# Optimization experiments

Measured on AMD Instinct MI355X. Metric: run time of the kernel, lower is better.

## Reference

```python
import jax, jax.numpy as jnp
import numpy as np

B, ND, NPR, D, H = 8, 512, 1024, 256, 8
DH = D // H
K_T, G_MIN, RHO, B_LAM, TOPK_RATIO, EDL_LAM = 4.0, 1e-4, 0.3, 0.01, 0.5, 1e-3
NEG = -1e30  # stands in for -inf in masked_fill (softmax weight is exactly 0 either way)


def setup_inputs():
    key = jax.random.key(0)
    ks = jax.random.split(key, 20)
    H_D = jax.random.normal(ks[0], (B, ND, D), jnp.float32)
    H_P = jax.random.normal(ks[1], (B, NPR, D), jnp.float32)
    mask_D = (jax.random.uniform(ks[2], (B, ND)) > 0.2).at[:, :2].set(True)
    mask_P = (jax.random.uniform(ks[3], (B, NPR)) > 0.2).at[:, :2].set(True)
    s = 0.02
    p = {
        'nig_w': s * jax.random.normal(ks[4], (D, 4), jnp.float32),
        'nig_b': jnp.zeros((4,), jnp.float32),
        'Wq': s * jax.random.normal(ks[5], (D, D), jnp.float32), 'bq': jnp.zeros((D,), jnp.float32),
        'Wk': s * jax.random.normal(ks[6], (D, D), jnp.float32), 'bk': jnp.zeros((D,), jnp.float32),
        'Wv': s * jax.random.normal(ks[7], (D, D), jnp.float32), 'bv': jnp.zeros((D,), jnp.float32),
        'Wo': s * jax.random.normal(ks[8], (D, D), jnp.float32), 'bo': jnp.zeros((D,), jnp.float32),
        'ln_g': jnp.ones((D,), jnp.float32), 'ln_b': jnp.zeros((D,), jnp.float32),
    }
    return dict(H_D=H_D, mask_D=mask_D, H_P=H_P, mask_P=mask_P, **p)


def _layernorm(x, g, b):
    m = jnp.mean(x, -1, keepdims=True)
    v = jnp.mean((x - m) ** 2, -1, keepdims=True)
    return (x - m) * jax.lax.rsqrt(v + 1e-5) * g + b


def _nig(h, w, b):
    # NIGHead: linear d->4 evidential params; s2 = predictive variance beta/(nu*(alpha-1))
    raw = h @ w + b                               # [B,N,4]
    nu = jax.nn.softplus(raw[..., 1])
    alpha = 1.0 + jax.nn.softplus(raw[..., 2])
    beta = jax.nn.softplus(raw[..., 3])
    s2 = beta / (nu * (alpha - 1.0) + 1e-6)
    return raw[..., 0], nu, alpha, beta, s2


def _apply_topk(g, mask):
    # per-row variable k = floor(clamp(sum(mask)*ratio, min=1)); keep top-k of g, zero rest
    k = jnp.maximum(jnp.sum(mask, axis=1).astype(jnp.float32) * TOPK_RATIO, 1.0).astype(jnp.int32)
    ranks = jnp.argsort(jnp.argsort(-g, axis=1), axis=1)  # rank 0 = largest
    keep = ranks < k[:, None]
    return jnp.where(keep, g, 0.0) * mask.astype(g.dtype)


def _mhca(qx, kx, mask_k, log_g, Wq, bq, Wk, bk, Wv, bv, Wo, bo, ln_g, ln_b):
    Bq, Nq, Dd = qx.shape
    Nk = kx.shape[1]
    q = (qx @ Wq + bq).reshape(Bq, Nq, H, DH).transpose(0, 2, 1, 3)
    k = (kx @ Wk + bk).reshape(Bq, Nk, H, DH).transpose(0, 2, 1, 3)
    v = (kx @ Wv + bv).reshape(Bq, Nk, H, DH).transpose(0, 2, 1, 3)
    attn = jnp.einsum('bhqd,bhkd->bhqk', q, k) / jnp.sqrt(jnp.float32(DH))
    attn = jnp.where(mask_k[:, None, None, :], attn, NEG)
    if log_g is not None:
        attn = attn + log_g[:, None, None, :]
    w = jax.nn.softmax(attn, axis=-1)
    ctx = jnp.einsum('bhqk,bhkd->bhqd', w, v).transpose(0, 2, 1, 3).reshape(Bq, Nq, Dd)
    return _layernorm(ctx @ Wo + bo + qx, ln_g, ln_b)


def reference(H_D, mask_D, H_P, mask_P, nig_w, nig_b, Wq, bq, Wk, bk, Wv, bv, Wo, bo, ln_g, ln_b):
    # stage='B', k_now=None path
    _, _, aD, bD, s2_D = _nig(H_D, nig_w, nig_b)
    _, _, aP, bP, s2_P = _nig(H_P, nig_w, nig_b)
    mDf, mPf = mask_D.astype(jnp.float32), mask_P.astype(jnp.float32)
    # GateFromUncertainty: g = clamp(exp(-k*s2), g_min, 1) * mask
    g_D = _apply_topk(jnp.clip(jnp.exp(-K_T * s2_D), G_MIN, 1.0) * mDf, mask_D)
    g_P = _apply_topk(jnp.clip(jnp.exp(-K_T * s2_P), G_MIN, 1.0) * mPf, mask_P)
    log_g_D, log_g_P = jnp.log(g_D + 1e-8), jnp.log(g_P + 1e-8)
    # BudgetRegularizer: lam*(masked mean gate - rho)^2 ; EDLRegularizer: lam*mean(alpha+beta)
    budget = lambda g, mf: B_LAM * (jnp.sum(g) / (jnp.sum(mf) + 1e-8) - RHO) ** 2
    edl = lambda a, b: EDL_LAM * jnp.mean(a + b)
    loss_reg = budget(g_D, mDf) + budget(g_P, mPf) + edl(aD, bD) + edl(aP, bP)
    mha = (Wq, bq, Wk, bk, Wv, bv, Wo, bo, ln_g, ln_b)
    Xd, Xp = H_D, H_P
    Xd = _mhca(Xd, Xp, mask_P, log_g_P, *mha)
    Xp = _mhca(Xp, Xd, mask_D, log_g_D, *mha)
    return Xd, Xp, g_D, g_P, loss_reg
```

## Files before the change

### kernel.cpp

```cpp
#include <hip/hip_runtime.h>
#include <hip/hip_bf16.h>
#include <math.h>

typedef __attribute__((ext_vector_type(8))) short s8;
typedef __attribute__((ext_vector_type(8))) unsigned short us8;
typedef __attribute__((ext_vector_type(4))) unsigned short us4;
typedef __attribute__((ext_vector_type(4))) float f4;

__device__ __forceinline__ unsigned short f2bf(float f) {
    unsigned int u = __float_as_uint(f);
    unsigned int r = u + 0x7FFFu + ((u >> 16) & 1u);
    return (unsigned short)(r >> 16);
}

__device__ __forceinline__ float softplus_f(float x) {
    return (x > 0.f) ? x + log1pf(expf(-x)) : log1pf(expf(x));
}

__global__ __launch_bounds__(256) void prep_nig_kernel(
        const float* __restrict__ W0, const float* __restrict__ W1,
        const float* __restrict__ W2, const float* __restrict__ W3,
        unsigned short* __restrict__ Wt,
        const float* __restrict__ H_D, const int* __restrict__ maskD,
        const float* __restrict__ H_P, const int* __restrict__ maskP,
        const float* __restrict__ nw, const float* __restrict__ nb,
        float* __restrict__ gpreD, float* __restrict__ gpreP,
        float* __restrict__ abD, float* __restrict__ abP,
        unsigned short* __restrict__ hdb, unsigned short* __restrict__ hpb) {
    int bx = blockIdx.x;
    if (bx < 256) {
        __shared__ float t[32][33];
        int wsel = bx >> 6, tile = bx & 63;
        const float* W = wsel == 0 ? W0 : wsel == 1 ? W1 : wsel == 2 ? W2 : W3;
        unsigned short* O = Wt + wsel * 65536;
        int k0 = (tile >> 3) * 32, n0 = (tile & 7) * 32;
        int r = threadIdx.x >> 5, c = threadIdx.x & 31;
#pragma unroll
        for (int i = 0; i < 4; ++i) t[r + i * 8][c] = W[(k0 + r + i * 8) * 256 + n0 + c];
        __syncthreads();
#pragma unroll
        for (int i = 0; i < 4; ++i) O[(n0 + r + i * 8) * 256 + k0 + c] = f2bf(t[c][r + i * 8]);
        return;
    }
    int row = (bx - 256) * 4 + (threadIdx.x >> 6);
    int lane = threadIdx.x & 63;
    const float* H; const int* mask; float* gpre; float* ab; unsigned short* hb; int lr;
    if (row < 4096) { H = H_D; mask = maskD; gpre = gpreD; ab = abD; hb = hdb; lr = row; }
    else            { H = H_P; mask = maskP; gpre = gpreP; ab = abP; hb = hpb; lr = row - 4096; }
    float4 hv = *(const float4*)(H + (size_t)lr * 256 + lane * 4);
    us4 h4 = { f2bf(hv.x), f2bf(hv.y), f2bf(hv.z), f2bf(hv.w) };
    *(us4*)&hb[(size_t)lr * 256 + lane * 4] = h4;
    float4 n0v = *(const float4*)&nw[(lane * 4 + 0) * 4];
    float4 n1v = *(const float4*)&nw[(lane * 4 + 1) * 4];
    float4 n2v = *(const float4*)&nw[(lane * 4 + 2) * 4];
    float4 n3v = *(const float4*)&nw[(lane * 4 + 3) * 4];
    float a1 = hv.x * n0v.y + hv.y * n1v.y + hv.z * n2v.y + hv.w * n3v.y;
    float a2 = hv.x * n0v.z + hv.y * n1v.z + hv.z * n2v.z + hv.w * n3v.z;
    float a3 = hv.x * n0v.w + hv.y * n1v.w + hv.z * n2v.w + hv.w * n3v.w;
#pragma unroll
    for (int o = 32; o; o >>= 1) {
        a1 += __shfl_xor(a1, o);
        a2 += __shfl_xor(a2, o);
        a3 += __shfl_xor(a3, o);
    }
    if (lane == 0) {
        float nu = softplus_f(a1 + nb[1]);
        float sa = softplus_f(a2 + nb[2]);
        float beta = softplus_f(a3 + nb[3]);
        float s2 = beta / (nu * sa + 1e-6f);
        float g = expf(-4.f * s2);
        g = fminf(fmaxf(g, 1e-4f), 1.f);
        gpre[lr] = (mask[lr] != 0) ? g : 0.f;
        ab[lr] = (1.f + sa) + beta;
    }
}

__device__ __forceinline__ void gemm64x128_lds(
        const unsigned short* __restrict__ Ab, const unsigned short* __restrict__ Wp,
        const float* __restrict__ bias, unsigned short* __restrict__ Cb,
        int idx, unsigned short (*bpan)[5120]) {
    const int tid = threadIdx.x, wid = tid >> 6, lane = tid & 63;
    const int g = lane >> 4, lo = lane & 15;
    const size_t row0 = (size_t)(idx >> 1) * 64 + wid * 16;
    const int n0 = (idx & 1) * 128;
    const int c0 = tid >> 2, q0 = tid & 3;
    const unsigned short* gp0 = Wp + (size_t)(n0 + c0) * 256 + q0 * 8;
    const unsigned short* gp1 = Wp + (size_t)(n0 + c0 + 64) * 256 + q0 * 8;
    const int l0 = c0 * 40 + q0 * 8;
    const int l1 = (c0 + 64) * 40 + q0 * 8;
    const unsigned short* ap = Ab + (row0 + lo) * 256 + g * 8;

    f4 acc[8];
#pragma unroll
    for (int f = 0; f < 8; ++f) acc[f] = (f4){0.f, 0.f, 0.f, 0.f};

    *(us8*)&bpan[0][l0] = *(const us8*)gp0;
    *(us8*)&bpan[0][l1] = *(const us8*)gp1;
    s8 av = *(const s8*)ap;

    for (int t = 0; t < 8; ++t) {
        const int buf = t & 1;
        us8 pn0, pn1; s8 avn;
        if (t < 7) {
            pn0 = *(const us8*)(gp0 + (t + 1) * 32);
            pn1 = *(const us8*)(gp1 + (t + 1) * 32);
            avn = *(const s8*)(ap + (t + 1) * 32);
        }
        __syncthreads();
#pragma unroll
        for (int f = 0; f < 8; ++f) {
            s8 bfr = *(const s8*)&bpan[buf][(f * 16 + lo) * 40 + g * 8];
            acc[f] = __builtin_amdgcn_mfma_f32_16x16x32_bf16(av, bfr, acc[f], 0, 0, 0);
        }
        if (t < 7) {
            *(us8*)&bpan[buf ^ 1][l0] = pn0;
            *(us8*)&bpan[buf ^ 1][l1] = pn1;
            av = avn;
        }
    }
#pragma unroll
    for (int f = 0; f < 8; ++f) {
        int col = n0 + f * 16 + lo;
        float bv2 = bias[col];
#pragma unroll
        for (int r = 0; r < 4; ++r)
            Cb[(row0 + g * 4 + r) * 256 + col] = f2bf(acc[f][r] + bv2);
    }
}

__device__ __forceinline__ void topk_body(
        const float* __restrict__ gpre, const int* __restrict__ mask,
        float* __restrict__ gout, float* __restrict__ logg,
        float* __restrict__ sgArr, float* __restrict__ smArr,
        int N, int b, int by, int bslot, float* grow, float* red) {
    int tid = threadIdx.x;
    int j = by * 256 + tid;
    for (int i = tid; i < N; i += 256) grow[i] = gpre[b * N + i];
    float cpart = 0.f;
    for (int i = tid; i < N; i += 256) cpart += (mask[b * N + i] != 0) ? 1.f : 0.f;
    red[tid] = cpart;
    __syncthreads();
    for (int s = 128; s; s >>= 1) { if (tid < s) red[tid] += red[tid + s]; __syncthreads(); }
    float count = red[0];
    __syncthreads();
    int k = (int)fmaxf(count * 0.5f, 1.0f);
    float gj = grow[j];
    int rank = 0;
    for (int i = 0; i < N; ++i) {
        float gi = grow[i];
        rank += (gi > gj || (gi == gj && i < j)) ? 1 : 0;
    }
    float gf = (rank < k) ? gj : 0.f;
    gout[b * N + j] = gf;
    logg[b * N + j] = logf(gf + 1e-8f);
    red[tid] = gf;
    __syncthreads();
    for (int s = 128; s; s >>= 1) { if (tid < s) red[tid] += red[tid + s]; __syncthreads(); }
    if (tid == 0) sgArr[bslot] = red[0];
    __syncthreads();
    red[tid] = (mask[b * N + j] != 0) ? 1.f : 0.f;
    __syncthreads();
    for (int s = 128; s; s >>= 1) { if (tid < s) red[tid] += red[tid + s]; __syncthreads(); }
    if (tid == 0) smArr[bslot] = red[0];
}

__global__ __launch_bounds__(256) void qkv_topk_kernel(
        const unsigned short* __restrict__ hdb, const unsigned short* __restrict__ hpb,
        const unsigned short* __restrict__ Wt,
        const float* __restrict__ bq, const float* __restrict__ bk, const float* __restrict__ bv,
        unsigned short* __restrict__ q1b, unsigned short* __restrict__ k1b,
        unsigned short* __restrict__ v1b, unsigned short* __restrict__ q2b,
        const float* __restrict__ gpreD, const int* __restrict__ maskD,
        float* __restrict__ goutD, float* __restrict__ loggD,
        const float* __restrict__ gpreP, const int* __restrict__ maskP,
        float* __restrict__ goutP, float* __restrict__ loggP,
        float* __restrict__ sgD, float* __restrict__ smD,
        float* __restrict__ sgP, float* __restrict__ smP,
        const float* __restrict__ abD, const float* __restrict__ abP,
        float* __restrict__ edl2) {
    __shared__ unsigned short bpan[2][5120];
    int bx = blockIdx.x;
    int tid = threadIdx.x;
    if (bx == 944) {
        float* red = (float*)&bpan[0][0];
        float s1 = 0.f, s2 = 0.f;
        for (int i = tid; i < 4096; i += 256) s1 += abD[i];
        for (int i = tid; i < 8192; i += 256) s2 += abP[i];
        red[tid] = s1;
        __syncthreads();
        for (int s = 128; s; s >>= 1) { if (tid < s) red[tid] += red[tid + s]; __syncthreads(); }
        if (tid == 0) edl2[0] = red[0];
        __syncthreads();
        red[tid] = s2;
        __syncthreads();
        for (int s = 128; s; s >>= 1) { if (tid < s) red[tid] += red[tid + s]; __syncthreads(); }
        if (tid == 0) edl2[1] = red[0];
        return;
    }
    if (bx >= 896) {
        float* grow = (float*)&bpan[0][0];
        float* red = grow + 1024;
        int tb = bx - 896;
        int b = tb & 7, by = tb >> 3;
        if (by < 2) topk_body(gpreD, maskD, goutD, loggD, sgD, smD, 512, b, by, b * 2 + by, grow, red);
        else        topk_body(gpreP, maskP, goutP, loggP, sgP, smP, 1024, b, by - 2, b * 4 + (by - 2), grow, red);
        return;
    }
    const unsigned short* Ab; const unsigned short* Wp; const float* bias;
    unsigned short* Cb; int idx;
    if (bx < 128)      { Ab = hdb; Wp = Wt;          bias = bq; Cb = q1b; idx = bx; }
    else if (bx < 384) { Ab = hpb; Wp = Wt + 65536;  bias = bk; Cb = k1b; idx = bx - 128; }
    else if (bx < 640) { Ab = hpb; Wp = Wt + 131072; bias = bv; Cb = v1b; idx = bx - 384; }
    else               { Ab = hpb; Wp = Wt;          bias = bq; Cb = q2b; idx = bx - 640; }
    gemm64x128_lds(Ab, Wp, bias, Cb, idx, bpan);
}

__global__ __launch_bounds__(256) void kv2_mega_kernel(
        const unsigned short* __restrict__ xdb, const unsigned short* __restrict__ Wt,
        const float* __restrict__ bk, const float* __restrict__ bv,
        unsigned short* __restrict__ k2b, unsigned short* __restrict__ v2b) {
    __shared__ unsigned short bpan[2][5120];
    int bx = blockIdx.x;
    const unsigned short* Wp; const float* bias; unsigned short* Cb; int idx;
    if (bx < 128) { Wp = Wt + 65536;  bias = bk; Cb = k2b; idx = bx; }
    else          { Wp = Wt + 131072; bias = bv; Cb = v2b; idx = bx - 128; }
    gemm64x128_lds(xdb, Wp, bias, Cb, idx, bpan);
}

__global__ __launch_bounds__(256) void gemm_o_ln_kernel(
        const unsigned short* __restrict__ A, const unsigned short* __restrict__ Wt,
        const float* __restrict__ bias, const float* __restrict__ resid,
        const float* __restrict__ gam, const float* __restrict__ bet,
        float* __restrict__ Out, unsigned short* __restrict__ OutB,
        const float* __restrict__ sgD, const float* __restrict__ smD,
        const float* __restrict__ sgP, const float* __restrict__ smP,
        const float* __restrict__ edl2, float* __restrict__ lossOut) {
    __shared__ float sums[4][16], sqs[4][16];
    const int tid = threadIdx.x, wid = tid >> 6, lane = tid & 63;
    const int g = lane >> 4, lo = lane & 15;
    const size_t row0 = (size_t)blockIdx.x * 16;
    const int c0 = wid * 64;
    f4 acc[4];
#pragma unroll
    for (int f = 0; f < 4; ++f) acc[f] = (f4){0.f, 0.f, 0.f, 0.f};
    for (int k0 = 0; k0 < 256; k0 += 32) {
        s8 af = *(const s8*)&A[(row0 + lo) * 256 + k0 + g * 8];
#pragma unroll
        for (int f = 0; f < 4; ++f) {
            s8 bfr = *(const s8*)&Wt[(size_t)(c0 + f * 16 + lo) * 256 + k0 + g * 8];
            acc[f] = __builtin_amdgcn_mfma_f32_16x16x32_bf16(af, bfr, acc[f], 0, 0, 0);
        }
    }
#pragma unroll
    for (int r = 0; r < 4; ++r) {
        size_t row = row0 + g * 4 + r;
        float sv = 0.f, qv = 0.f;
#pragma unroll
        for (int f = 0; f < 4; ++f) {
            int col = c0 + f * 16 + lo;
            float v = acc[f][r] + bias[col] + resid[row * 256 + col];
            acc[f][r] = v;
            sv += v;
            qv += v * v;
        }
#pragma unroll
        for (int o = 1; o < 16; o <<= 1) { sv += __shfl_xor(sv, o); qv += __shfl_xor(qv, o); }
        if (lo == 0) { sums[wid][g * 4 + r] = sv; sqs[wid][g * 4 + r] = qv; }
    }
    __syncthreads();
#pragma unroll
    for (int r = 0; r < 4; ++r) {
        int rl = g * 4 + r;
        size_t row = row0 + rl;
        float st = sums[0][rl] + sums[1][rl] + sums[2][rl] + sums[3][rl];
        float qt = sqs[0][rl] + sqs[1][rl] + sqs[2][rl] + sqs[3][rl];
        float mean = st * (1.f / 256.f);
        float var = qt * (1.f / 256.f) - mean * mean;
        float inv = rsqrtf(var + 1e-5f);
#pragma unroll
        for (int f = 0; f < 4; ++f) {
            int col = c0 + f * 16 + lo;
            float y = (acc[f][r] - mean) * inv * gam[col] + bet[col];
            Out[row * 256 + col] = y;
            if (OutB) OutB[row * 256 + col] = f2bf(y);
        }
    }
    if (lossOut && blockIdx.x == 0 && tid < 64) {
        float sgd = 0.f, smd = 0.f, sgp = 0.f, smp = 0.f;
        if (lane < 16) { sgd = sgD[lane]; smd = smD[lane]; }
        if (lane < 32) { sgp = sgP[lane]; smp = smP[lane]; }
#pragma unroll
        for (int o = 16; o; o >>= 1) { sgp += __shfl_xor(sgp, o); smp += __shfl_xor(smp, o); }
#pragma unroll
        for (int o = 8; o; o >>= 1) { sgd += __shfl_xor(sgd, o); smd += __shfl_xor(smd, o); }
        if (lane == 0) {
            float t1 = sgd / (smd + 1e-8f) - 0.3f;
            float t2 = sgp / (smp + 1e-8f) - 0.3f;
            lossOut[0] = 0.01f * (t1 * t1) + 0.01f * (t2 * t2)
                       + 1e-3f * (edl2[0] / 4096.f) + 1e-3f * (edl2[1] / 8192.f);
        }
    }
}

template <int NK>
__global__ __launch_bounds__(256) void attn_mfma_kernel(
        const unsigned short* __restrict__ qb, const unsigned short* __restrict__ kb,
        const unsigned short* __restrict__ vb, const float* __restrict__ logg,
        unsigned short* __restrict__ ctxb, int Nq) {
    __shared__ unsigned short Kf[2][2048];
    __shared__ unsigned short Vf[2][2048];
    __shared__ unsigned short Pf[4][1152];
    __shared__ float lg[2][64];
    constexpr int NT = NK / 64;

    const int tid = threadIdx.x;
    const int wid = tid >> 6, lane = tid & 63;
    const int g = lane >> 4, lo = lane & 15;
    const int b = blockIdx.y >> 3, h = blockIdx.y & 7;
    const int q0 = blockIdx.x * 64 + wid * 16;
    const size_t bq = (size_t)b * Nq, bk = (size_t)b * NK;
    const float scale = 0.17677669529663687f;

    const int kloc = tid >> 2, quad = tid & 3;
    const size_t gbase = (bk + kloc) * 256 + h * 32 + quad * 8;
    const int kfa = ((kloc >> 4) << 9) + (quad * 16 + (kloc & 15)) * 8;
    const int vkh = kloc >> 5, vgg = (kloc >> 3) & 3, vj = kloc & 7;
    const int vdh = quad >> 1, vl0 = (quad & 1) * 8;
    const int vb0 = ((vkh * 2 + vdh) << 9) + vgg * 128 + vj;

    s8 qf = *(const s8*)&qb[(bq + q0 + lo) * 256 + h * 32 + g * 8];

    f4 o0 = {0.f, 0.f, 0.f, 0.f}, o1 = {0.f, 0.f, 0.f, 0.f};
    float mrow[4] = {-3e38f, -3e38f, -3e38f, -3e38f};
    float lsum[4] = {0.f, 0.f, 0.f, 0.f};

    us8 kreg = *(const us8*)&kb[gbase];
    us8 vreg = *(const us8*)&vb[gbase];
    float lgreg = (tid < 64) ? logg[bk + tid] : 0.f;
    *(us8*)&Kf[0][kfa] = kreg;
#pragma unroll
    for (int jj = 0; jj < 8; ++jj) Vf[0][vb0 + (vl0 + jj) * 8] = vreg[jj];
    if (tid < 64) lg[0][tid] = lgreg;

    for (int t = 0; t < NT; ++t) {
        const int cur = t & 1;
        if (t + 1 < NT) {
            size_t ga = gbase + (size_t)(t + 1) * 64 * 256;
            kreg = *(const us8*)&kb[ga];
            vreg = *(const us8*)&vb[ga];
            if (tid < 64) lgreg = logg[bk + (t + 1) * 64 + tid];
        }
        __syncthreads();

        f4 sc[4];
#pragma unroll
        for (int ks = 0; ks < 4; ++ks) {
            s8 kfr = *(const s8*)&Kf[cur][(ks << 9) + lane * 8];
            f4 z = {0.f, 0.f, 0.f, 0.f};
            f4 s4 = __builtin_amdgcn_mfma_f32_16x16x32_bf16(qf, kfr, z, 0, 0, 0);
            float lga = lg[cur][ks * 16 + lo];
#pragma unroll
            for (int r = 0; r < 4; ++r) sc[ks][r] = s4[r] * scale + lga;
        }
        float vm[4];
#pragma unroll
        for (int r = 0; r < 4; ++r)
            vm[r] = fmaxf(fmaxf(sc[0][r], sc[1][r]), fmaxf(sc[2][r], sc[3][r]));
#pragma unroll
        for (int off = 1; off < 16; off <<= 1)
#pragma unroll
            for (int r = 0; r < 4; ++r) vm[r] = fmaxf(vm[r], __shfl_xor(vm[r], off));
        float al[4], ps[4];
#pragma unroll
        for (int r = 0; r < 4; ++r) {
            float mn = fmaxf(mrow[r], vm[r]);
            al[r] = __expf(mrow[r] - mn);
            mrow[r] = mn;
            ps[r] = 0.f;
        }
#pragma unroll
        for (int ks = 0; ks < 4; ++ks)
#pragma unroll
            for (int r = 0; r < 4; ++r) {
                float p = __expf(sc[ks][r] - mrow[r]);
                ps[r] += p;
                Pf[wid][(g * 4 + r) * 72 + ks * 16 + lo] = f2bf(p);
            }
#pragma unroll
        for (int off = 1; off < 16; off <<= 1)
#pragma unroll
            for (int r = 0; r < 4; ++r) ps[r] += __shfl_xor(ps[r], off);
#pragma unroll
        for (int r = 0; r < 4; ++r) {
            lsum[r] = lsum[r] * al[r] + ps[r];
            o0[r] *= al[r];
            o1[r] *= al[r];
        }
#pragma unroll
        for (int kh = 0; kh < 2; ++kh) {
            s8 pfr = *(const s8*)&Pf[wid][lo * 72 + kh * 32 + g * 8];
            s8 vf0 = *(const s8*)&Vf[cur][((kh * 2 + 0) << 9) + lane * 8];
            o0 = __builtin_amdgcn_mfma_f32_16x16x32_bf16(pfr, vf0, o0, 0, 0, 0);
            s8 vf1 = *(const s8*)&Vf[cur][((kh * 2 + 1) << 9) + lane * 8];
            o1 = __builtin_amdgcn_mfma_f32_16x16x32_bf16(pfr, vf1, o1, 0, 0, 0);
        }
        if (t + 1 < NT) {
            const int nxt = cur ^ 1;
            *(us8*)&Kf[nxt][kfa] = kreg;
#pragma unroll
            for (int jj = 0; jj < 8; ++jj) Vf[nxt][vb0 + (vl0 + jj) * 8] = vreg[jj];
            if (tid < 64) lg[nxt][tid] = lgreg;
        }
    }
#pragma unroll
    for (int r = 0; r < 4; ++r) {
        float inv = 1.f / lsum[r];
        unsigned short* cp = ctxb + (bq + q0 + g * 4 + r) * 256 + h * 32;
        cp[lo] = f2bf(o0[r] * inv);
        cp[16 + lo] = f2bf(o1[r] * inv);
    }
}

extern "C" void kernel_launch(void* const* d_in, const int* in_sizes, int n_in,
                              void* d_out, int out_size, void* d_ws, size_t ws_size,
                              hipStream_t stream) {
    (void)in_sizes; (void)n_in; (void)out_size; (void)ws_size;
    const float* H_D   = (const float*)d_in[0];
    const int*   maskD = (const int*)d_in[1];
    const float* H_P   = (const float*)d_in[2];
    const int*   maskP = (const int*)d_in[3];
    const float* nig_w = (const float*)d_in[4];
    const float* nig_b = (const float*)d_in[5];
    const float* Wq = (const float*)d_in[6];
    const float* bq = (const float*)d_in[7];
    const float* Wk = (const float*)d_in[8];
    const float* bk = (const float*)d_in[9];
    const float* Wv = (const float*)d_in[10];
    const float* bv = (const float*)d_in[11];
    const float* Wo = (const float*)d_in[12];
    const float* bo = (const float*)d_in[13];
    const float* ln_g = (const float*)d_in[14];
    const float* ln_b = (const float*)d_in[15];
    float* out = (float*)d_out;
    float* ws = (float*)d_ws;

    float* outXd = out + 0;
    float* outXp = out + 1048576;
    float* outGD = out + 3145728;
    float* outGP = out + 3149824;
    float* outLo = out + 3158016;

    float* abD   = ws;
    float* abP   = ws + 4096;
    float* sgD   = ws + 12288;
    float* smD   = ws + 12304;
    float* sgP   = ws + 12320;
    float* smP   = ws + 12352;
    float* edl2  = ws + 12384;
    float* gpreD = ws + 12416;
    float* gpreP = ws + 16512;
    float* logD  = ws + 24704;
    float* logP  = ws + 28800;
    unsigned short* ub  = (unsigned short*)(ws + 36992);
    unsigned short* Wt  = ub;
    unsigned short* q1b = ub + 262144;
    unsigned short* k1b = ub + 1310720;
    unsigned short* v1b = ub + 3407872;
    unsigned short* q2b = ub + 5505024;
    unsigned short* c1b = ub + 7602176;
    unsigned short* xdb = ub + 8650752;
    unsigned short* k2b = ub + 9699328;
    unsigned short* v2b = ub + 10747904;
    unsigned short* c2b = ub + 11796480;
    unsigned short* hdb = c1b;
    unsigned short* hpb = xdb;

    prep_nig_kernel<<<3328, 256, 0, stream>>>(Wq, Wk, Wv, Wo, Wt,
                                              H_D, maskD, H_P, maskP,
                                              nig_w, nig_b, gpreD, gpreP, abD, abP,
                                              hdb, hpb);
    qkv_topk_kernel<<<945, 256, 0, stream>>>(hdb, hpb, Wt, bq, bk, bv,
                                             q1b, k1b, v1b, q2b,
                                             gpreD, maskD, outGD, logD,
                                             gpreP, maskP, outGP, logP,
                                             sgD, smD, sgP, smP, abD, abP, edl2);
    attn_mfma_kernel<1024><<<dim3(8, 64), 256, 0, stream>>>(q1b, k1b, v1b, logP, c1b, 512);
    gemm_o_ln_kernel<<<256, 256, 0, stream>>>(c1b, Wt + 3 * 65536, bo, H_D, ln_g, ln_b,
                                              outXd, xdb, nullptr, nullptr, nullptr, nullptr,
                                              nullptr, nullptr);
    kv2_mega_kernel<<<256, 256, 0, stream>>>(xdb, Wt, bk, bv, k2b, v2b);
    attn_mfma_kernel<512><<<dim3(16, 64), 256, 0, stream>>>(q2b, k2b, v2b, logD, c2b, 1024);
    gemm_o_ln_kernel<<<512, 256, 0, stream>>>(c2b, Wt + 3 * 65536, bo, H_P, ln_g, ln_b,
                                              outXp, nullptr, sgD, smD, sgP, smP, edl2, outLo);
}
```

Baseline: 140.2 us.

## Fuse Xd output projection+LayerNorm with the K/V projection for the second attention

The first output-projection+LayerNorm kernel now stages its bf16 normalized rows in LDS and immediately computes the K and V projections for the second attention pass from them. This removes one kernel launch and the global write and re-read of the intermediate bf16 Xd buffer. The fused kernel uses only 256 blocks of 16 rows each and reads the Wk/Wv weights directly from global memory per block instead of through the LDS-panelled 64x128 GEMM, so it has less parallelism and more weight traffic.

```diff
diff --git a/kernel.cpp b/kernel.cpp
--- a/kernel.cpp
+++ b/kernel.cpp
@@ -215,23 +215,98 @@
     gemm64x128_lds(Ab, Wp, bias, Cb, idx, bpan);
 }
 
-__global__ __launch_bounds__(256) void kv2_mega_kernel(
-        const unsigned short* __restrict__ xdb, const unsigned short* __restrict__ Wt,
+__global__ __launch_bounds__(256) void gemm_o_ln_kv2_kernel(
+        const unsigned short* __restrict__ A, const unsigned short* __restrict__ Wt,
+        const float* __restrict__ bo, const float* __restrict__ resid,
+        const float* __restrict__ gam, const float* __restrict__ bet,
+        float* __restrict__ Out,
         const float* __restrict__ bk, const float* __restrict__ bv,
         unsigned short* __restrict__ k2b, unsigned short* __restrict__ v2b) {
-    __shared__ unsigned short bpan[2][5120];
-    int bx = blockIdx.x;
-    const unsigned short* Wp; const float* bias; unsigned short* Cb; int idx;
-    if (bx < 128) { Wp = Wt + 65536;  bias = bk; Cb = k2b; idx = bx; }
-    else          { Wp = Wt + 131072; bias = bv; Cb = v2b; idx = bx - 128; }
-    gemm64x128_lds(xdb, Wp, bias, Cb, idx, bpan);
+    __shared__ float sums[4][16], sqs[4][16];
+    __shared__ unsigned short xs[16][264];
+    const int tid = threadIdx.x, wid = tid >> 6, lane = tid & 63;
+    const int g = lane >> 4, lo = lane & 15;
+    const size_t row0 = (size_t)blockIdx.x * 16;
+    const int c0 = wid * 64;
+    const unsigned short* Wo = Wt + 3 * 65536;
+    f4 acc[4];
+#pragma unroll
+    for (int f = 0; f < 4; ++f) acc[f] = (f4){0.f, 0.f, 0.f, 0.f};
+    for (int k0 = 0; k0 < 256; k0 += 32) {
+        s8 af = *(const s8*)&A[(row0 + lo) * 256 + k0 + g * 8];
+#pragma unroll
+        for (int f = 0; f < 4; ++f) {
+            s8 bfr = *(const s8*)&Wo[(size_t)(c0 + f * 16 + lo) * 256 + k0 + g * 8];
+            acc[f] = __builtin_amdgcn_mfma_f32_16x16x32_bf16(af, bfr, acc[f], 0, 0, 0);
+        }
+    }
+#pragma unroll
+    for (int r = 0; r < 4; ++r) {
+        size_t row = row0 + g * 4 + r;
+        float sv = 0.f, qv = 0.f;
+#pragma unroll
+        for (int f = 0; f < 4; ++f) {
+            int col = c0 + f * 16 + lo;
+            float v = acc[f][r] + bo[col] + resid[row * 256 + col];
+            acc[f][r] = v;
+            sv += v;
+            qv += v * v;
+        }
+#pragma unroll
+        for (int o = 1; o < 16; o <<= 1) { sv += __shfl_xor(sv, o); qv += __shfl_xor(qv, o); }
+        if (lo == 0) { sums[wid][g * 4 + r] = sv; sqs[wid][g * 4 + r] = qv; }
+    }
+    __syncthreads();
+#pragma unroll
+    for (int r = 0; r < 4; ++r) {
+        int rl = g * 4 + r;
+        size_t row = row0 + rl;
+        float st = sums[0][rl] + sums[1][rl] + sums[2][rl] + sums[3][rl];
+        float qt = sqs[0][rl] + sqs[1][rl] + sqs[2][rl] + sqs[3][rl];
+        float mean = st * (1.f / 256.f);
+        float var = qt * (1.f / 256.f) - mean * mean;
+        float inv = rsqrtf(var + 1e-5f);
+#pragma unroll
+        for (int f = 0; f < 4; ++f) {
+            int col = c0 + f * 16 + lo;
+            float y = (acc[f][r] - mean) * inv * gam[col] + bet[col];
+            Out[row * 256 + col] = y;
+            xs[rl][col] = f2bf(y);
+        }
+    }
+    __syncthreads();
+#pragma unroll
+    for (int w = 0; w < 2; ++w) {
+        const unsigned short* Wp = Wt + (w ? 2 : 1) * 65536;
+        const float* bias = w ? bv : bk;
+        unsigned short* Cb = w ? v2b : k2b;
+        f4 a2[4];
+#pragma unroll
+        for (int f = 0; f < 4; ++f) a2[f] = (f4){0.f, 0.f, 0.f, 0.f};
+        for (int k0 = 0; k0 < 256; k0 += 32) {
+            s8 af = *(const s8*)&xs[lo][k0 + g * 8];
+#pragma unroll
+            for (int f = 0; f < 4; ++f) {
+                s8 bfr = *(const s8*)&Wp[(size_t)(c0 + f * 16 + lo) * 256 + k0 + g * 8];
+                a2[f] = __builtin_amdgcn_mfma_f32_16x16x32_bf16(af, bfr, a2[f], 0, 0, 0);
+            }
+        }
+#pragma unroll
+        for (int f = 0; f < 4; ++f) {
+            int col = c0 + f * 16 + lo;
+            float bv2 = bias[col];
+#pragma unroll
+            for (int r = 0; r < 4; ++r)
+                Cb[(row0 + g * 4 + r) * 256 + col] = f2bf(a2[f][r] + bv2);
+        }
+    }
 }
 
 __global__ __launch_bounds__(256) void gemm_o_ln_kernel(
         const unsigned short* __restrict__ A, const unsigned short* __restrict__ Wt,
         const float* __restrict__ bias, const float* __restrict__ resid,
         const float* __restrict__ gam, const float* __restrict__ bet,
-        float* __restrict__ Out, unsigned short* __restrict__ OutB,
+        float* __restrict__ Out,
         const float* __restrict__ sgD, const float* __restrict__ smD,
         const float* __restrict__ sgP, const float* __restrict__ smP,
         const float* __restrict__ edl2, float* __restrict__ lossOut) {
@@ -280,9 +355,7 @@
 #pragma unroll
         for (int f = 0; f < 4; ++f) {
             int col = c0 + f * 16 + lo;
-            float y = (acc[f][r] - mean) * inv * gam[col] + bet[col];
-            Out[row * 256 + col] = y;
-            if (OutB) OutB[row * 256 + col] = f2bf(y);
+            Out[row * 256 + col] = (acc[f][r] - mean) * inv * gam[col] + bet[col];
         }
     }
     if (lossOut && blockIdx.x == 0 && tid < 64) {
@@ -468,12 +541,11 @@
     unsigned short* v1b = ub + 3407872;
     unsigned short* q2b = ub + 5505024;
     unsigned short* c1b = ub + 7602176;
-    unsigned short* xdb = ub + 8650752;
-    unsigned short* k2b = ub + 9699328;
-    unsigned short* v2b = ub + 10747904;
-    unsigned short* c2b = ub + 11796480;
+    unsigned short* k2b = ub + 8650752;
+    unsigned short* v2b = ub + 9699328;
+    unsigned short* c2b = ub + 10747904;
     unsigned short* hdb = c1b;
-    unsigned short* hpb = xdb;
+    unsigned short* hpb = k2b;
 
     prep_nig_kernel<<<3328, 256, 0, stream>>>(Wq, Wk, Wv, Wo, Wt,
                                               H_D, maskD, H_P, maskP,
@@ -485,11 +557,9 @@
                                              gpreP, maskP, outGP, logP,
                                              sgD, smD, sgP, smP, abD, abP, edl2);
     attn_mfma_kernel<1024><<<dim3(8, 64), 256, 0, stream>>>(q1b, k1b, v1b, logP, c1b, 512);
-    gemm_o_ln_kernel<<<256, 256, 0, stream>>>(c1b, Wt + 3 * 65536, bo, H_D, ln_g, ln_b,
-                                              outXd, xdb, nullptr, nullptr, nullptr, nullptr,
-                                              nullptr, nullptr);
-    kv2_mega_kernel<<<256, 256, 0, stream>>>(xdb, Wt, bk, bv, k2b, v2b);
+    gemm_o_ln_kv2_kernel<<<256, 256, 0, stream>>>(c1b, Wt, bo, H_D, ln_g, ln_b,
+                                                  outXd, bk, bv, k2b, v2b);
     attn_mfma_kernel<512><<<dim3(16, 64), 256, 0, stream>>>(q2b, k2b, v2b, logD, c2b, 1024);
     gemm_o_ln_kernel<<<512, 256, 0, stream>>>(c2b, Wt + 3 * 65536, bo, H_P, ln_g, ln_b,
-                                              outXp, nullptr, sgD, smD, sgP, smP, edl2, outLo);
-}
+                                              outXp, sgD, smD, sgP, smP, edl2, outLo);
+}
```

After: 141.7 us. No clear change (+1.1%).
